# Performance work log

Measured on AMD Instinct MI355X. Metric: run time of the kernel, lower is better.

The kernel has to match this reference:

```python
import jax, jax.numpy as jnp
import numpy as np

B, T, D, H = 4, 2048, 1024, 16
DH = D // H

def setup_inputs() -> dict:
    key = jax.random.key(0)
    k1, k2, k3 = jax.random.split(key, 3)
    x = jax.random.normal(k1, (B, T, D), dtype=jnp.float32)
    w_qkv = jax.random.normal(k2, (D, 3 * D), dtype=jnp.float32) * (1.0 / np.sqrt(D))
    w_out = jax.random.normal(k3, (D, D), dtype=jnp.float32) * (1.0 / np.sqrt(D))
    return {"x": x, "w_qkv": w_qkv, "w_out": w_out}

def reference(x, w_qkv, w_out):
    Bq, Tq, C = x.shape
    qkv = x @ w_qkv                                   # [B,T,3D]
    q, k, v = jnp.split(qkv, 3, axis=-1)
    q = q.reshape(Bq, Tq, H, DH).transpose(0, 2, 1, 3)  # [B,H,T,dh]
    k = k.reshape(Bq, Tq, H, DH).transpose(0, 2, 1, 3)
    v = v.reshape(Bq, Tq, H, DH).transpose(0, 2, 1, 3)
    scores = jnp.einsum('bhqd,bhkd->bhqk', q, k) / jnp.sqrt(jnp.float32(DH))
    mask = jnp.tril(jnp.ones((Tq, Tq), dtype=bool))
    scores = jnp.where(mask, scores, jnp.float32(-jnp.inf))
    attn = jax.nn.softmax(scores, axis=-1)
    out = jnp.einsum('bhqk,bhkd->bhqd', attn, v)      # [B,H,T,dh]
    out = out.transpose(0, 2, 1, 3).reshape(Bq, Tq, C)
    return out @ w_out
```

## Files before the change

kernel.cpp:

```cpp
#include <hip/hip_runtime.h>

#define B_ 4
#define T_ 2048
#define D_ 1024
#define H_ 16
#define DH_ 64
#define BH_ (B_*H_)
#define M_ (B_*T_)
#define N3_ (3*D_)

typedef __attribute__((ext_vector_type(8))) __bf16 bf16x8;
typedef __attribute__((ext_vector_type(4))) float f32x4;
typedef __attribute__((ext_vector_type(16))) float f32x16;
typedef __attribute__((ext_vector_type(8))) unsigned short u16x8;
typedef __attribute__((ext_vector_type(4))) unsigned short u16x4;
typedef int i32x2 __attribute__((ext_vector_type(2)));

__device__ inline void gload_lds16(const void* g, void* l) {
  __builtin_amdgcn_global_load_lds((const __attribute__((address_space(1))) void*)g,
                                   (__attribute__((address_space(3))) void*)l, 16, 0, 0);
}

__device__ inline unsigned short f2bf(float v) {
  __bf16 t = (__bf16)v;
  return *(unsigned short*)&t;
}

__device__ inline unsigned pk2(float lo, float hi2) {
  return (unsigned)f2bf(lo) | ((unsigned)f2bf(hi2) << 16);
}

template<int BASE>
__device__ inline bf16x8 buildP(const f32x16& S) {
  unsigned a = pk2(S[BASE+0], S[BASE+1]);
  unsigned b = pk2(S[BASE+2], S[BASE+3]);
  unsigned c = pk2(S[BASE+4], S[BASE+5]);
  unsigned d = pk2(S[BASE+6], S[BASE+7]);
  i32x2 r0 = __builtin_amdgcn_permlane32_swap((int)a, (int)c, false, false);
  i32x2 r1 = __builtin_amdgcn_permlane32_swap((int)b, (int)d, false, false);
  union { unsigned u[4]; bf16x8 v; } U;
  U.u[0] = (unsigned)r0[0];
  U.u[1] = (unsigned)r1[0];
  U.u[2] = (unsigned)r0[1];
  U.u[3] = (unsigned)r1[1];
  return U.v;
}

__global__ void prep(const float* __restrict__ x, unsigned short* __restrict__ xb,
                     const float* __restrict__ wq, unsigned short* __restrict__ wqT,
                     const float* __restrict__ wo, unsigned short* __restrict__ woT) {
  __shared__ unsigned short lds[64][72];
  int bid = blockIdx.x, tid = threadIdx.x;
  if (bid < 4096) {
    int i = bid * 256 + tid;
    const float4* p = (const float4*)(x + (size_t)i * 8);
    float4 a = p[0], b = p[1];
    float v[8] = {a.x, a.y, a.z, a.w, b.x, b.y, b.z, b.w};
    u16x8 r;
#pragma unroll
    for (int j = 0; j < 8; ++j) r[j] = f2bf(v[j]);
    *(u16x8*)(xb + (size_t)i * 8) = r;
    return;
  }
  const float* w;
  unsigned short* wt;
  int n0, k0, Ndim;
  if (bid < 4096 + 768) {
    int b2 = bid - 4096;
    w = wq; wt = wqT; Ndim = N3_;
    n0 = (b2 % 48) * 64; k0 = (b2 / 48) * 64;
  } else {
    int b3 = bid - 4864;
    w = wo; wt = woT; Ndim = D_;
    n0 = (b3 % 16) * 64; k0 = (b3 / 16) * 64;
  }
#pragma unroll
  for (int i = 0; i < 2; ++i) {
    int idx = i * 256 + tid;
    int r = idx >> 3, c8 = idx & 7;
    const float4* src = (const float4*)(w + (size_t)(k0 + r) * Ndim + n0 + c8 * 8);
    float4 a = src[0], b = src[1];
    float v[8] = {a.x, a.y, a.z, a.w, b.x, b.y, b.z, b.w};
#pragma unroll
    for (int j = 0; j < 8; ++j) lds[r][c8 * 8 + j] = f2bf(v[j]);
  }
  __syncthreads();
#pragma unroll
  for (int i = 0; i < 2; ++i) {
    int idx = i * 256 + tid;
    int r = idx >> 3, c8 = idx & 7;
    u16x8 o;
#pragma unroll
    for (int j = 0; j < 8; ++j) o[j] = lds[c8 * 8 + j][r];
    *(u16x8*)(wt + (size_t)(n0 + r) * 1024 + k0 + c8 * 8) = o;
  }
}

__global__ __launch_bounds__(256) void gemm2b(
    const unsigned short* __restrict__ A,
    const unsigned short* __restrict__ BT,
    int epi,
    unsigned short* __restrict__ qb, unsigned short* __restrict__ kb, unsigned short* __restrict__ vtb,
    float* __restrict__ outf) {
  extern __shared__ __align__(16) char lds[];
  const int tid = threadIdx.x;
  const int wave = tid >> 6, lane = tid & 63, g = lane >> 4, c = lane & 15;
  const int wm = wave >> 1, wn = wave & 1;
  int flat = blockIdx.y * gridDim.x + blockIdx.x;
  int xcd = flat & 7, local = flat >> 3;
  int bx = xcd * 8 + (local & 7);
  int by = local >> 3;
  const int m0 = bx * 128, n0 = by * 128;

  f32x4 acc[4][4] = {};

  auto stage = [&](int slot, int jj) {
    char* sb = lds + slot * 32768;
#pragma unroll
    for (int i = 0; i < 4; ++i) {
      int idx = i * 256 + tid;
      int r = idx >> 3, s = idx & 7;
      gload_lds16(A + (size_t)(m0 + r) * 1024 + jj * 64 + 8 * (s ^ (r & 7)),
                  sb + idx * 16);
    }
#pragma unroll
    for (int i = 0; i < 4; ++i) {
      int idx = i * 256 + tid;
      int r = idx >> 3, s = idx & 7;
      gload_lds16(BT + (size_t)(n0 + r) * 1024 + jj * 64 + 8 * (s ^ (r & 7)),
                  sb + 16384 + idx * 16);
    }
  };

  stage(0, 0);
  for (int j = 0; j < 16; ++j) {
    if (j < 15) {
      stage((j + 1) & 1, j + 1);
      asm volatile("s_waitcnt vmcnt(8)" ::: "memory");
    } else {
      asm volatile("s_waitcnt vmcnt(0)" ::: "memory");
    }
    __builtin_amdgcn_s_barrier();
    asm volatile("" ::: "memory");

    const char* sA = lds + (j & 1) * 32768;
    const char* sB = sA + 16384;
#pragma unroll
    for (int kc = 0; kc < 2; ++kc) {
      bf16x8 af[4], bf[4];
#pragma unroll
      for (int mt = 0; mt < 4; ++mt) {
        int r = wm * 64 + mt * 16 + c;
        af[mt] = *(const bf16x8*)(sA + r * 128 + 16 * ((kc * 4 + g) ^ (r & 7)));
      }
#pragma unroll
      for (int nt = 0; nt < 4; ++nt) {
        int r = wn * 64 + nt * 16 + c;
        bf[nt] = *(const bf16x8*)(sB + r * 128 + 16 * ((kc * 4 + g) ^ (r & 7)));
      }
      __builtin_amdgcn_s_setprio(1);
#pragma unroll
      for (int mt = 0; mt < 4; ++mt)
#pragma unroll
        for (int nt = 0; nt < 4; ++nt)
          acc[mt][nt] = __builtin_amdgcn_mfma_f32_16x16x32_bf16(af[mt], bf[nt], acc[mt][nt], 0, 0, 0);
      __builtin_amdgcn_s_setprio(0);
    }

    __builtin_amdgcn_s_barrier();
    asm volatile("" ::: "memory");
  }

  if (epi == 0) {
    int which = n0 >> 10;
    int colbase = n0 - (which << 10);
    if (which == 2) {
#pragma unroll
      for (int mt = 0; mt < 4; ++mt)
#pragma unroll
        for (int nt = 0; nt < 4; ++nt) {
          int m = m0 + wm * 64 + mt * 16 + g * 4;
          int n = colbase + wn * 64 + nt * 16 + c;
          int b = m >> 11, t = m & 2047;
          int h = n >> 6, d = n & 63;
          u16x4 pk;
#pragma unroll
          for (int i = 0; i < 4; ++i) pk[i] = f2bf(acc[mt][nt][i]);
          *(u16x4*)(vtb + ((size_t)(b * H_ + h) * 64 + d) * T_ + t) = pk;
        }
    } else {
      unsigned short* dst = which == 0 ? qb : kb;
      float scale = which == 0 ? 0.18033688011112042f : 1.0f;
#pragma unroll
      for (int mt = 0; mt < 4; ++mt)
#pragma unroll
        for (int nt = 0; nt < 4; ++nt)
#pragma unroll
          for (int i = 0; i < 4; ++i) {
            int m = m0 + wm * 64 + mt * 16 + g * 4 + i;
            int n = colbase + wn * 64 + nt * 16 + c;
            int b = m >> 11, t = m & 2047;
            int h = n >> 6, d = n & 63;
            dst[(((size_t)(b * H_ + h) * T_ + t) << 6) + d] = f2bf(acc[mt][nt][i] * scale);
          }
    }
  } else {
#pragma unroll
    for (int mt = 0; mt < 4; ++mt)
#pragma unroll
      for (int nt = 0; nt < 4; ++nt)
#pragma unroll
        for (int i = 0; i < 4; ++i) {
          int m = m0 + wm * 64 + mt * 16 + g * 4 + i;
          int n = n0 + wn * 64 + nt * 16 + c;
          outf[(size_t)m * 1024 + n] = acc[mt][nt][i];
        }
  }
}

#define PV_STEP(PF, KC)                                                                \
  {                                                                                    \
    bf16x8 pf = (PF);                                                                  \
    int dr0 = q32, dr1 = 32 + q32;                                                     \
    bf16x8 v0 = *(const bf16x8*)(sV + dr0 * 128 + 16 * (((KC)*2 + hi) ^ (dr0 & 7)));   \
    bf16x8 v1 = *(const bf16x8*)(sV + dr1 * 128 + 16 * (((KC)*2 + hi) ^ (dr1 & 7)));   \
    oT0 = __builtin_amdgcn_mfma_f32_32x32x16_bf16(v0, pf, oT0, 0, 0, 0);               \
    oT1 = __builtin_amdgcn_mfma_f32_32x32x16_bf16(v1, pf, oT1, 0, 0, 0);               \
  }

__global__ __launch_bounds__(512) void attn(
    const unsigned short* __restrict__ qbp,
    const unsigned short* __restrict__ kb,
    const unsigned short* __restrict__ vt,
    unsigned short* __restrict__ ao) {
  __shared__ __align__(16) char pool[49152];
  const int tid = threadIdx.x;
  const int wave = tid >> 6, lane = tid & 63;
  const int q32 = lane & 31, hi = lane >> 5;
  const int bh = blockIdx.y;
  const int flip = (bh >> 5) & 1;
  const int pb = flip ? blockIdx.x : (T_ / 256 - 1) - blockIdx.x;
  const int q0w = pb * 256 + wave * 32;
  const int kmax = 4 * pb + 3;
  const int dtile = 4 * pb + (wave >> 1);

  bf16x8 qf[4];
#pragma unroll
  for (int dhc = 0; dhc < 4; ++dhc)
    qf[dhc] = *(const bf16x8*)(qbp + ((size_t)bh * T_ + q0w + q32) * 64 + dhc * 16 + hi * 8);

  f32x16 oT0 = {}, oT1 = {};
  float l_run = 0.0f;

  auto stage = [&](int buf, int kt) {
    int r = tid >> 3, s8 = tid & 7;
    gload_lds16(kb + ((size_t)bh * T_ + kt * 64 + r) * 64 + 8 * (s8 ^ (r & 7)),
                pool + buf * 16384 + tid * 16);
    gload_lds16(vt + ((size_t)bh * 64 + r) * T_ + kt * 64 + 8 * (s8 ^ (r & 7)),
                pool + buf * 16384 + 8192 + tid * 16);
  };

  stage(0, 0);
  stage(1, 1);
  int sj = 0;
  for (int kt = 0; kt <= kmax; ++kt) {
    asm volatile("s_waitcnt vmcnt(2)" ::: "memory");
    __builtin_amdgcn_s_barrier();
    asm volatile("" ::: "memory");
    int st2 = sj + 2; if (st2 >= 3) st2 -= 3;
    if (kt + 2 <= kmax) stage(st2, kt + 2);
    if (kt <= dtile) {
      const char* sK = pool + sj * 16384;
      const char* sV = sK + 8192;

      f32x16 st0 = {}, st1 = {};
      __builtin_amdgcn_s_setprio(1);
#pragma unroll
      for (int dhc = 0; dhc < 4; ++dhc) {
        int kr0 = q32, kr1 = 32 + q32;
        bf16x8 k0 = *(const bf16x8*)(sK + kr0 * 128 + 16 * ((dhc * 2 + hi) ^ (kr0 & 7)));
        bf16x8 k1 = *(const bf16x8*)(sK + kr1 * 128 + 16 * ((dhc * 2 + hi) ^ (kr1 & 7)));
        st0 = __builtin_amdgcn_mfma_f32_32x32x16_bf16(k0, qf[dhc], st0, 0, 0, 0);
        st1 = __builtin_amdgcn_mfma_f32_32x32x16_bf16(k1, qf[dhc], st1, 0, 0, 0);
      }
      __builtin_amdgcn_s_setprio(0);

      if (kt == dtile) {
        int qg = q0w + q32;
#pragma unroll
        for (int r = 0; r < 16; ++r) {
          int krow = kt * 64 + (r & 3) + 8 * (r >> 2) + 4 * hi;
          if (krow > qg) st0[r] = -INFINITY;
          if (krow + 32 > qg) st1[r] = -INFINITY;
        }
      }

      float ps0 = 0.0f, ps1 = 0.0f, ps2 = 0.0f, ps3 = 0.0f;
#pragma unroll
      for (int r = 0; r < 16; r += 4) {
        float a0 = __builtin_amdgcn_exp2f(st0[r + 0]); st0[r + 0] = a0; ps0 += a0;
        float a1 = __builtin_amdgcn_exp2f(st0[r + 1]); st0[r + 1] = a1; ps1 += a1;
        float a2 = __builtin_amdgcn_exp2f(st0[r + 2]); st0[r + 2] = a2; ps2 += a2;
        float a3 = __builtin_amdgcn_exp2f(st0[r + 3]); st0[r + 3] = a3; ps3 += a3;
      }
#pragma unroll
      for (int r = 0; r < 16; r += 4) {
        float a0 = __builtin_amdgcn_exp2f(st1[r + 0]); st1[r + 0] = a0; ps0 += a0;
        float a1 = __builtin_amdgcn_exp2f(st1[r + 1]); st1[r + 1] = a1; ps1 += a1;
        float a2 = __builtin_amdgcn_exp2f(st1[r + 2]); st1[r + 2] = a2; ps2 += a2;
        float a3 = __builtin_amdgcn_exp2f(st1[r + 3]); st1[r + 3] = a3; ps3 += a3;
      }
      float ps = (ps0 + ps1) + (ps2 + ps3);
      ps += __shfl_xor(ps, 32);
      l_run += ps;

      __builtin_amdgcn_s_setprio(1);
      PV_STEP(buildP<0>(st0), 0)
      PV_STEP(buildP<8>(st0), 1)
      PV_STEP(buildP<0>(st1), 2)
      PV_STEP(buildP<8>(st1), 3)
      __builtin_amdgcn_s_setprio(0);
    }
    sj = sj + 1; if (sj >= 3) sj -= 3;
  }

  __syncthreads();
  unsigned short* ep = (unsigned short*)pool + wave * (32 * 72);
  float inv_l = 1.0f / l_run;
#pragma unroll
  for (int r = 0; r < 16; ++r) {
    int d0 = (r & 3) + 8 * (r >> 2) + 4 * hi;
    ep[q32 * 72 + d0]      = f2bf(oT0[r] * inv_l);
    ep[q32 * 72 + 32 + d0] = f2bf(oT1[r] * inv_l);
  }
  __syncthreads();
  {
    int q = lane >> 1, half = lane & 1;
    int t = q0w + q;
    int b = bh >> 4, h = bh & 15;
    const unsigned short* row = ep + q * 72 + half * 32;
    unsigned short* g = ao + ((size_t)(b * T_ + t)) * 1024 + h * 64 + half * 32;
#pragma unroll
    for (int j = 0; j < 4; ++j)
      *(u16x8*)(g + j * 8) = *(const u16x8*)(row + j * 8);
  }
}

extern "C" void kernel_launch(void* const* d_in, const int* in_sizes, int n_in,
                              void* d_out, int out_size, void* d_ws, size_t ws_size,
                              hipStream_t stream) {
  const float* x = (const float*)d_in[0];
  const float* w_qkv = (const float*)d_in[1];
  const float* w_out = (const float*)d_in[2];
  float* out = (float*)d_out;

  char* ws = (char*)d_ws;
  size_t off = 0;
  auto alloc = [&](size_t bytes) {
    char* p = ws + off;
    off += (bytes + 255) & ~(size_t)255;
    return p;
  };
  unsigned short* xb    = (unsigned short*)alloc((size_t)M_ * D_ * 2);
  unsigned short* wqkvT = (unsigned short*)alloc((size_t)N3_ * D_ * 2);
  unsigned short* woutT = (unsigned short*)alloc((size_t)D_ * D_ * 2);
  unsigned short* qbuf  = (unsigned short*)alloc((size_t)BH_ * T_ * 64 * 2);
  unsigned short* kbuf  = (unsigned short*)alloc((size_t)BH_ * T_ * 64 * 2);
  unsigned short* vtb   = (unsigned short*)alloc((size_t)BH_ * 64 * T_ * 2);
  unsigned short* ao    = xb;

  hipFuncSetAttribute(reinterpret_cast<const void*>(gemm2b),
                      hipFuncAttributeMaxDynamicSharedMemorySize, 65536);

  prep<<<4096 + 768 + 256, 256, 0, stream>>>(x, xb, w_qkv, wqkvT, w_out, woutT);
  gemm2b<<<dim3(M_ / 128, N3_ / 128), 256, 65536, stream>>>(xb, wqkvT, 0, qbuf, kbuf, vtb, nullptr);
  attn<<<dim3(T_ / 256, BH_), 512, 0, stream>>>(qbuf, kbuf, vtb, ao);
  gemm2b<<<dim3(M_ / 128, D_ / 128), 256, 65536, stream>>>(ao, woutT, 1, nullptr, nullptr, nullptr, out);
}
```

Before: 148.9 us.

## Split KV range of longest causal attention blocks and merge with combine kernel

```diff
diff --git a/kernel.cpp b/kernel.cpp
--- a/kernel.cpp
+++ b/kernel.cpp
@@ -24,6 +24,11 @@
 __device__ inline unsigned short f2bf(float v) {
   __bf16 t = (__bf16)v;
   return *(unsigned short*)&t;
+}
+
+__device__ inline float bf2f(unsigned short u) {
+  unsigned x = ((unsigned)u) << 16;
+  return __builtin_bit_cast(float, x);
 }
 
 __device__ inline unsigned pk2(float lo, float hi2) {
@@ -232,16 +237,29 @@
     const unsigned short* __restrict__ qbp,
     const unsigned short* __restrict__ kb,
     const unsigned short* __restrict__ vt,
-    unsigned short* __restrict__ ao) {
+    unsigned short* __restrict__ ao,
+    unsigned short* __restrict__ opart,
+    float* __restrict__ lpart) {
   __shared__ __align__(16) char pool[49152];
   const int tid = threadIdx.x;
   const int wave = tid >> 6, lane = tid & 63;
   const int q32 = lane & 31, hi = lane >> 5;
   const int bh = blockIdx.y;
-  const int flip = (bh >> 5) & 1;
-  const int pb = flip ? blockIdx.x : (T_ / 256 - 1) - blockIdx.x;
+
+  int u;
+  switch (blockIdx.x) {
+    case 0: u = 5; break; case 1: u = 4; break; case 2: u = 3; break;
+    case 3: u = 8; break; case 4: u = 9; break; case 5: u = 6; break;
+    case 6: u = 7; break; case 7: u = 2; break; case 8: u = 1; break;
+    default: u = 0; break;
+  }
+  int pb, k0t, nt, pidx;
+  bool part;
+  if (u < 6)      { pb = u; k0t = 0;            nt = 4 * u + 4; part = false; pidx = 0; }
+  else if (u < 8) { pb = 6; k0t = 14 * (u - 6); nt = 14; part = true; pidx = (bh * 2 + 0) * 2 + (u - 6); }
+  else            { pb = 7; k0t = 16 * (u - 8); nt = 16; part = true; pidx = (bh * 2 + 1) * 2 + (u - 8); }
+  const int k1t = k0t + nt - 1;
   const int q0w = pb * 256 + wave * 32;
-  const int kmax = 4 * pb + 3;
   const int dtile = 4 * pb + (wave >> 1);
 
   bf16x8 qf[4];
@@ -260,15 +278,15 @@
                 pool + buf * 16384 + 8192 + tid * 16);
   };
 
-  stage(0, 0);
-  stage(1, 1);
+  stage(0, k0t);
+  stage(1, k0t + 1);
   int sj = 0;
-  for (int kt = 0; kt <= kmax; ++kt) {
+  for (int kt = k0t; kt <= k1t; ++kt) {
     asm volatile("s_waitcnt vmcnt(2)" ::: "memory");
     __builtin_amdgcn_s_barrier();
     asm volatile("" ::: "memory");
     int st2 = sj + 2; if (st2 >= 3) st2 -= 3;
-    if (kt + 2 <= kmax) stage(st2, kt + 2);
+    if (kt + 2 <= k1t) stage(st2, kt + 2);
     if (kt <= dtile) {
       const char* sK = pool + sj * 16384;
       const char* sV = sK + 8192;
@@ -326,7 +344,8 @@
 
   __syncthreads();
   unsigned short* ep = (unsigned short*)pool + wave * (32 * 72);
-  float inv_l = 1.0f / l_run;
+  float inv_l = part ? 1.0f : (1.0f / l_run);
+  if (part && hi == 0) lpart[pidx * 256 + wave * 32 + q32] = l_run;
 #pragma unroll
   for (int r = 0; r < 16; ++r) {
     int d0 = (r & 3) + 8 * (r >> 2) + 4 * hi;
@@ -336,13 +355,51 @@
   __syncthreads();
   {
     int q = lane >> 1, half = lane & 1;
-    int t = q0w + q;
-    int b = bh >> 4, h = bh & 15;
     const unsigned short* row = ep + q * 72 + half * 32;
-    unsigned short* g = ao + ((size_t)(b * T_ + t)) * 1024 + h * 64 + half * 32;
+    unsigned short* g;
+    if (part) {
+      g = opart + ((size_t)pidx * 256 + wave * 32 + q) * 64 + half * 32;
+    } else {
+      int t = q0w + q;
+      int b = bh >> 4, h = bh & 15;
+      g = ao + ((size_t)(b * T_ + t)) * 1024 + h * 64 + half * 32;
+    }
 #pragma unroll
     for (int j = 0; j < 4; ++j)
       *(u16x8*)(g + j * 8) = *(const u16x8*)(row + j * 8);
+  }
+}
+
+__global__ __launch_bounds__(256) void combine(
+    const unsigned short* __restrict__ opart, const float* __restrict__ lpart,
+    unsigned short* __restrict__ ao) {
+  int pair = blockIdx.x;
+  int bh = pair >> 1, pb = 6 + (pair & 1);
+  int tid = threadIdx.x;
+  int rloc = tid >> 2, dc = tid & 3;
+  const unsigned short* A = opart + ((size_t)(pair * 2 + 0)) * 256 * 64;
+  const unsigned short* Bp = opart + ((size_t)(pair * 2 + 1)) * 256 * 64;
+  const float* lA = lpart + (pair * 2 + 0) * 256;
+  const float* lB = lpart + (pair * 2 + 1) * 256;
+  int b = bh >> 4, hh = bh & 15;
+#pragma unroll
+  for (int rr = 0; rr < 4; ++rr) {
+    int row = rr * 64 + rloc;
+    float inv = 1.0f / (lA[row] + lB[row]);
+    const unsigned short* pa = A + row * 64 + dc * 16;
+    const unsigned short* pbp = Bp + row * 64 + dc * 16;
+    u16x8 a0 = *(const u16x8*)pa, a1 = *(const u16x8*)(pa + 8);
+    u16x8 b0 = *(const u16x8*)pbp, b1 = *(const u16x8*)(pbp + 8);
+    u16x8 o0, o1;
+#pragma unroll
+    for (int j = 0; j < 8; ++j) {
+      o0[j] = f2bf((bf2f(a0[j]) + bf2f(b0[j])) * inv);
+      o1[j] = f2bf((bf2f(a1[j]) + bf2f(b1[j])) * inv);
+    }
+    int t = pb * 256 + row;
+    unsigned short* g = ao + ((size_t)(b * T_ + t)) * 1024 + hh * 64 + dc * 16;
+    *(u16x8*)g = o0;
+    *(u16x8*)(g + 8) = o1;
   }
 }
 
@@ -367,6 +424,8 @@
   unsigned short* qbuf  = (unsigned short*)alloc((size_t)BH_ * T_ * 64 * 2);
   unsigned short* kbuf  = (unsigned short*)alloc((size_t)BH_ * T_ * 64 * 2);
   unsigned short* vtb   = (unsigned short*)alloc((size_t)BH_ * 64 * T_ * 2);
+  unsigned short* opart = (unsigned short*)alloc((size_t)256 * 256 * 64 * 2);
+  float*          lpart = (float*)alloc((size_t)256 * 256 * 4);
   unsigned short* ao    = xb;
 
   hipFuncSetAttribute(reinterpret_cast<const void*>(gemm2b),
@@ -374,6 +433,7 @@
 
   prep<<<4096 + 768 + 256, 256, 0, stream>>>(x, xb, w_qkv, wqkvT, w_out, woutT);
   gemm2b<<<dim3(M_ / 128, N3_ / 128), 256, 65536, stream>>>(xb, wqkvT, 0, qbuf, kbuf, vtb, nullptr);
-  attn<<<dim3(T_ / 256, BH_), 512, 0, stream>>>(qbuf, kbuf, vtb, ao);
+  attn<<<dim3(10, BH_), 512, 0, stream>>>(qbuf, kbuf, vtb, ao, opart, lpart);
+  combine<<<128, 256, 0, stream>>>(opart, lpart, ao);
   gemm2b<<<dim3(M_ / 128, D_ / 128), 256, 65536, stream>>>(ao, woutT, 1, nullptr, nullptr, nullptr, out);
 }
```

Result: slower. 164.7 us (+10.7%).
